# Performance work log

Hardware: AMD Instinct MI355X
Metric: run time of the kernel (lower is better)

Reference implementation:

```python
import jax, jax.numpy as jnp
import numpy as np

LOG_INV_TEMP = float(np.log(1.0 / 0.07))
B, N_IMG, N_GPS, G_DIM = 256, 49, 32, 256


def setup_inputs() -> dict:
    key = jax.random.key(0)
    k1, k2 = jax.random.split(key)
    return {
        "image_g_tokens": jax.random.normal(k1, (B, N_IMG, G_DIM), dtype=jnp.float32),
        "gps_g_tokens": jax.random.normal(k2, (B, N_GPS, G_DIM), dtype=jnp.float32),
        "logit_scale": jnp.asarray(LOG_INV_TEMP, dtype=jnp.float32),
    }


def _l2norm(x, eps=1e-12):
    # matches F.normalize(p=2, dim=-1)
    n = jnp.sqrt(jnp.sum(x * x, axis=-1, keepdims=True))
    return x / jnp.maximum(n, eps)


def _ce(logits, labels):
    # mean cross-entropy with integer labels
    logz = jax.nn.logsumexp(logits, axis=1)
    picked = jnp.take_along_axis(logits, labels[:, None], axis=1)[:, 0]
    return jnp.mean(logz - picked)


def reference(image_g_tokens, gps_g_tokens, logit_scale):
    img = _l2norm(image_g_tokens)   # (B, n, d)
    gps = _l2norm(gps_g_tokens)     # (B, m, d)
    # dist not initialized -> gather is identity, global == local
    scale = jnp.minimum(jnp.exp(logit_scale), 100.0)

    # token-level max-sim: (B, G, n, m) pairwise similarities
    sims_i2g = jnp.einsum('bnd,gmd->bgnm', img, gps)
    sims_g2i = jnp.einsum('bmd,gnd->bgmn', gps, img)
    logits_i2g = jnp.mean(jnp.max(sims_i2g, axis=3), axis=2) * scale  # (B, G)
    logits_g2i = jnp.mean(jnp.max(sims_g2i, axis=3), axis=2) * scale  # (B, G)

    labels = jnp.arange(img.shape[0])
    loss = (_ce(logits_i2g, labels) + _ce(logits_g2i, labels)) / 2.0
    return loss
```

## Files before the change

### kernel.cpp

```cpp
#include <hip/hip_runtime.h>

#define BB   256
#define NIMG 49
#define NGPS 32
#define DIM  256
#define MPAD 64

typedef __attribute__((ext_vector_type(8))) __bf16 bf16x8;
typedef __attribute__((ext_vector_type(4))) float  f32x4;
typedef __attribute__((ext_vector_type(4))) unsigned int u32x4;

__device__ inline unsigned short f2bf(float f) {
  unsigned int u = __float_as_uint(f);
  u += 0x7fff + ((u >> 16) & 1);
  return (unsigned short)(u >> 16);
}

template<int CTRL>
__device__ inline float dppmax(float v) {
  float o = __int_as_float(__builtin_amdgcn_update_dpp(0, __float_as_int(v), CTRL, 0xF, 0xF, true));
  return fmaxf(v, o);
}
template<int CTRL>
__device__ inline float dppadd(float v) {
  float o = __int_as_float(__builtin_amdgcn_update_dpp(0, __float_as_int(v), CTRL, 0xF, 0xF, true));
  return v + o;
}
__device__ inline float max16(float v) {
  v = dppmax<0xB1>(v); v = dppmax<0x4E>(v); v = dppmax<0x141>(v); v = dppmax<0x140>(v);
  return v;
}
__device__ inline float sum16(float v) {
  v = dppadd<0xB1>(v); v = dppadd<0x4E>(v); v = dppadd<0x141>(v); v = dppadd<0x140>(v);
  return v;
}

__global__ __launch_bounds__(256) void norm_kernel(
    const float* __restrict__ img, const float* __restrict__ gps,
    unsigned short* __restrict__ imgS, unsigned short* __restrict__ gpsS)
{
  int w    = (blockIdx.x * 256 + threadIdx.x) >> 6;
  int lane = threadIdx.x & 63;

  f32x4 x = (f32x4){0.f, 0.f, 0.f, 0.f};
  bool isimg; int b = 0, n = 0, g = 0, m = 0;
  if (w < BB * MPAD) {
    isimg = true; b = w >> 6; n = w & 63;
    if (n < NIMG)
      x = *reinterpret_cast<const f32x4*>(img + ((size_t)b * NIMG + n) * DIM + lane * 4);
  } else {
    isimg = false; int t = w - BB * MPAD; g = t >> 5; m = t & 31;
    x = *reinterpret_cast<const f32x4*>(gps + (size_t)t * DIM + lane * 4);
  }

  float ss = x[0]*x[0] + x[1]*x[1] + x[2]*x[2] + x[3]*x[3];
  #pragma unroll
  for (int d = 1; d < 64; d <<= 1) ss += __shfl_xor(ss, d);
  float inv = (ss > 0.f) ? (1.0f / fmaxf(sqrtf(ss), 1e-12f)) : 0.f;

  unsigned int w01 = (unsigned)f2bf(x[0]*inv) | ((unsigned)f2bf(x[1]*inv) << 16);
  unsigned int w23 = (unsigned)f2bf(x[2]*inv) | ((unsigned)f2bf(x[3]*inv) << 16);

  int L = lane;
  unsigned int a0 = __shfl(w01, 2 * L);
  unsigned int a1 = __shfl(w23, 2 * L);
  unsigned int a2 = __shfl(w01, 2 * L + 1);
  unsigned int a3 = __shfl(w23, 2 * L + 1);
  if (L < 32) {
    u32x4 v = {a0, a1, a2, a3};
    unsigned short* dst;
    if (isimg) {
      dst = imgS + (size_t)b * 16384 + L * 512 + n * 8;
    } else {
      int mt = m >> 4, c = m & 15, kc = L >> 2, grp = L & 3;
      dst = gpsS + (size_t)g * 8192 + mt * 4096 + kc * 512 + (grp * 16 + c) * 8;
    }
    *reinterpret_cast<u32x4*>(dst) = v;
  }
}

__global__ __launch_bounds__(256, 4) void pair_kernel(
    const unsigned short* __restrict__ imgS, const unsigned short* __restrict__ gpsS,
    float* __restrict__ i2g, float* __restrict__ g2i)
{
  int tid  = threadIdx.x;
  int wv   = tid >> 6;
  int lane = tid & 63;
  int c    = lane & 15, grp = lane >> 4;
  int b    = blockIdx.x >> 3, gc = blockIdx.x & 7;
  int wvu  = __builtin_amdgcn_readfirstlane(wv);

  __shared__ unsigned short As[MPAD * DIM];

  {
    const unsigned short* src = imgS + (size_t)b * 16384 + lane * 8;
    #pragma unroll
    for (int i = 0; i < 8; ++i) {
      int s = wvu * 8 + i;
      bf16x8 v = *reinterpret_cast<const bf16x8*>(src + s * 512);
      unsigned int rb = lane * 512;
      unsigned int sw = (lane & 7) << 4;
      *reinterpret_cast<bf16x8*>(reinterpret_cast<char*>(As) + ((rb + s * 16) ^ sw)) = v;
    }
  }
  __syncthreads();

  const char* Ab = reinterpret_cast<const char*>(As);
  unsigned int swr   = (c & 7) << 4;
  unsigned int abase = c * 512;

  const unsigned short* gb = gpsS + ((size_t)(gc * 32 + wvu * 8)) * 8192;
  unsigned int lane8 = lane * 8;

  #pragma unroll 1
  for (int st = 0; st < 4; ++st) {
    f32x4 acc[2][2][4];
    #pragma unroll
    for (int g = 0; g < 2; ++g)
      #pragma unroll
      for (int mt = 0; mt < 2; ++mt)
        #pragma unroll
        for (int hf = 0; hf < 4; ++hf)
          acc[g][mt][hf] = (f32x4){0.f, 0.f, 0.f, 0.f};

    #pragma unroll 2
    for (int kc = 0; kc < 8; ++kc) {
      const unsigned short* p = gb + kc * 512 + lane8;
      bf16x8 q00 = *reinterpret_cast<const bf16x8*>(p);
      bf16x8 q01 = *reinterpret_cast<const bf16x8*>(p + 4096);
      bf16x8 q10 = *reinterpret_cast<const bf16x8*>(p + 8192);
      bf16x8 q11 = *reinterpret_cast<const bf16x8*>(p + 12288);
      unsigned int off = ((unsigned)(grp * 16 + kc * 64)) ^ swr;
      const char* ab = Ab + abase + off;
      bf16x8 a0 = *reinterpret_cast<const bf16x8*>(ab);
      bf16x8 a1 = *reinterpret_cast<const bf16x8*>(ab + 8192);
      bf16x8 a2 = *reinterpret_cast<const bf16x8*>(ab + 16384);
      bf16x8 a3 = *reinterpret_cast<const bf16x8*>(ab + 24576);
      acc[0][0][0] = __builtin_amdgcn_mfma_f32_16x16x32_bf16(q00, a0, acc[0][0][0], 0, 0, 0);
      acc[0][0][1] = __builtin_amdgcn_mfma_f32_16x16x32_bf16(q00, a1, acc[0][0][1], 0, 0, 0);
      acc[0][0][2] = __builtin_amdgcn_mfma_f32_16x16x32_bf16(q00, a2, acc[0][0][2], 0, 0, 0);
      acc[0][0][3] = __builtin_amdgcn_mfma_f32_16x16x32_bf16(q00, a3, acc[0][0][3], 0, 0, 0);
      acc[0][1][0] = __builtin_amdgcn_mfma_f32_16x16x32_bf16(q01, a0, acc[0][1][0], 0, 0, 0);
      acc[0][1][1] = __builtin_amdgcn_mfma_f32_16x16x32_bf16(q01, a1, acc[0][1][1], 0, 0, 0);
      acc[0][1][2] = __builtin_amdgcn_mfma_f32_16x16x32_bf16(q01, a2, acc[0][1][2], 0, 0, 0);
      acc[0][1][3] = __builtin_amdgcn_mfma_f32_16x16x32_bf16(q01, a3, acc[0][1][3], 0, 0, 0);
      acc[1][0][0] = __builtin_amdgcn_mfma_f32_16x16x32_bf16(q10, a0, acc[1][0][0], 0, 0, 0);
      acc[1][0][1] = __builtin_amdgcn_mfma_f32_16x16x32_bf16(q10, a1, acc[1][0][1], 0, 0, 0);
      acc[1][0][2] = __builtin_amdgcn_mfma_f32_16x16x32_bf16(q10, a2, acc[1][0][2], 0, 0, 0);
      acc[1][0][3] = __builtin_amdgcn_mfma_f32_16x16x32_bf16(q10, a3, acc[1][0][3], 0, 0, 0);
      acc[1][1][0] = __builtin_amdgcn_mfma_f32_16x16x32_bf16(q11, a0, acc[1][1][0], 0, 0, 0);
      acc[1][1][1] = __builtin_amdgcn_mfma_f32_16x16x32_bf16(q11, a1, acc[1][1][1], 0, 0, 0);
      acc[1][1][2] = __builtin_amdgcn_mfma_f32_16x16x32_bf16(q11, a2, acc[1][1][2], 0, 0, 0);
      acc[1][1][3] = __builtin_amdgcn_mfma_f32_16x16x32_bf16(q11, a3, acc[1][1][3], 0, 0, 0);
    }

    #pragma unroll
    for (int g = 0; g < 2; ++g) {
      float vmax[4];
      #pragma unroll
      for (int hf = 0; hf < 4; ++hf) {
        float m0 = fmaxf(fmaxf(acc[g][0][hf][0], acc[g][0][hf][1]),
                         fmaxf(acc[g][0][hf][2], acc[g][0][hf][3]));
        float m1 = fmaxf(fmaxf(acc[g][1][hf][0], acc[g][1][hf][1]),
                         fmaxf(acc[g][1][hf][2], acc[g][1][hf][3]));
        float vm = fmaxf(m0, m1);
        vm = fmaxf(vm, __shfl_xor(vm, 16));
        vm = fmaxf(vm, __shfl_xor(vm, 32));
        vmax[hf] = vm;
      }
      float s = vmax[0] + vmax[1] + vmax[2] + ((c == 0) ? vmax[3] : 0.0f);
      s = sum16(s);

      float t = 0.f;
      #pragma unroll
      for (int mt = 0; mt < 2; ++mt)
        #pragma unroll
        for (int r = 0; r < 4; ++r) {
          float h3 = (c == 0) ? acc[g][mt][3][r] : -1.0e30f;
          float hm = fmaxf(fmaxf(acc[g][mt][0][r], acc[g][mt][1][r]),
                           fmaxf(acc[g][mt][2][r], h3));
          hm = max16(hm);
          t += hm;
        }
      t += __shfl_xor(t, 16);
      t += __shfl_xor(t, 32);

      if (lane == 0) {
        int gg = gc * 32 + wvu * 8 + st * 2 + g;
        i2g[b * 256 + gg] = s * (1.0f / NIMG);
        g2i[gg * 256 + b] = t * (1.0f / NGPS);
      }
    }
    gb += 16384;
  }
}

__global__ __launch_bounds__(256) void ce_kernel(
    const float* __restrict__ i2g, const float* __restrict__ g2i,
    const float* __restrict__ lsp, float* __restrict__ partial)
{
  int b = blockIdx.x, t = threadIdx.x, lane = t & 63, wv = t >> 6;
  float s = fminf(expf(lsp[0]), 100.0f);
  float v1 = s * i2g[b * 256 + t];
  float v2 = s * g2i[b * 256 + t];

  float m1 = v1, m2 = v2;
  #pragma unroll
  for (int d = 1; d < 64; d <<= 1) {
    m1 = fmaxf(m1, __shfl_xor(m1, d));
    m2 = fmaxf(m2, __shfl_xor(m2, d));
  }
  __shared__ float sm[2][4];
  if (lane == 0) { sm[0][wv] = m1; sm[1][wv] = m2; }
  __syncthreads();
  m1 = fmaxf(fmaxf(sm[0][0], sm[0][1]), fmaxf(sm[0][2], sm[0][3]));
  m2 = fmaxf(fmaxf(sm[1][0], sm[1][1]), fmaxf(sm[1][2], sm[1][3]));

  float e1 = expf(v1 - m1), e2 = expf(v2 - m2);
  #pragma unroll
  for (int d = 1; d < 64; d <<= 1) {
    e1 += __shfl_xor(e1, d);
    e2 += __shfl_xor(e2, d);
  }
  __shared__ float se[2][4];
  if (lane == 0) { se[0][wv] = e1; se[1][wv] = e2; }
  __syncthreads();
  if (t == 0) {
    float S1 = se[0][0] + se[0][1] + se[0][2] + se[0][3];
    float S2 = se[1][0] + se[1][1] + se[1][2] + se[1][3];
    float lse1 = m1 + logf(S1);
    float lse2 = m2 + logf(S2);
    partial[b] = (lse1 - s * i2g[b * 257]) + (lse2 - s * g2i[b * 257]);
  }
}

__global__ __launch_bounds__(256) void finish_kernel(
    const float* __restrict__ partial, float* __restrict__ out)
{
  int t = threadIdx.x, lane = t & 63, wv = t >> 6;
  float v = partial[t];
  #pragma unroll
  for (int d = 1; d < 64; d <<= 1) v += __shfl_xor(v, d);
  __shared__ float sp[4];
  if (lane == 0) sp[wv] = v;
  __syncthreads();
  if (t == 0) out[0] = (sp[0] + sp[1] + sp[2] + sp[3]) * (1.0f / 512.0f);
}

extern "C" void kernel_launch(void* const* d_in, const int* in_sizes, int n_in,
                              void* d_out, int out_size, void* d_ws, size_t ws_size,
                              hipStream_t stream)
{
  const float* img = (const float*)d_in[0];
  const float* gps = (const float*)d_in[1];
  const float* lsp = (const float*)d_in[2];
  float* out = (float*)d_out;
  char* ws = (char*)d_ws;

  unsigned short* imgS = (unsigned short*)(ws);
  unsigned short* gpsS = (unsigned short*)(ws + 8388608);
  float* i2g     = (float*)(ws + 12582912);
  float* g2i     = (float*)(ws + 12845056);
  float* partial = (float*)(ws + 13107200);

  norm_kernel<<<6144, 256, 0, stream>>>(img, gps, imgS, gpsS);
  pair_kernel<<<2048, 256, 0, stream>>>(imgS, gpsS, i2g, g2i);
  ce_kernel<<<256, 256, 0, stream>>>(i2g, g2i, lsp, partial);
  finish_kernel<<<1, 256, 0, stream>>>(partial, out);
}
```

Before: 87.09 us.

## Store image tokens in MFMA fragment layout and load directly from global

The normalization kernel now writes image tokens in a pre-swizzled MFMA operand layout. The pair kernel can then read A fragments straight from global memory (L2/L1) instead of staging a 32KB tile in LDS behind a barrier. This removes the LDS fill, the __syncthreads and the LDS reads. In exchange every wave re-reads the image tile from cache. The launch-bounds occupancy hint drops from 4 to 3 blocks per CU to give more register room for the extra in-flight global loads.

```diff
diff --git a/kernel.cpp b/kernel.cpp
--- a/kernel.cpp
+++ b/kernel.cpp
@@ -37,7 +37,7 @@
 
 __global__ __launch_bounds__(256) void norm_kernel(
     const float* __restrict__ img, const float* __restrict__ gps,
-    unsigned short* __restrict__ imgS, unsigned short* __restrict__ gpsS)
+    unsigned short* __restrict__ imgA, unsigned short* __restrict__ gpsS)
 {
   int w    = (blockIdx.x * 256 + threadIdx.x) >> 6;
   int lane = threadIdx.x & 63;
@@ -70,7 +70,8 @@
     u32x4 v = {a0, a1, a2, a3};
     unsigned short* dst;
     if (isimg) {
-      dst = imgS + (size_t)b * 16384 + L * 512 + n * 8;
+      dst = imgA + (size_t)b * 16384 + (L >> 2) * 2048 + (n >> 4) * 512
+                 + ((L & 3) * 16 + (n & 15)) * 8;
     } else {
       int mt = m >> 4, c = m & 15, kc = L >> 2, grp = L & 3;
       dst = gpsS + (size_t)g * 8192 + mt * 4096 + kc * 512 + (grp * 16 + c) * 8;
@@ -79,8 +80,8 @@
   }
 }
 
-__global__ __launch_bounds__(256, 4) void pair_kernel(
-    const unsigned short* __restrict__ imgS, const unsigned short* __restrict__ gpsS,
+__global__ __launch_bounds__(256, 3) void pair_kernel(
+    const unsigned short* __restrict__ imgA, const unsigned short* __restrict__ gpsS,
     float* __restrict__ i2g, float* __restrict__ g2i)
 {
   int tid  = threadIdx.x;
@@ -90,27 +91,9 @@
   int b    = blockIdx.x >> 3, gc = blockIdx.x & 7;
   int wvu  = __builtin_amdgcn_readfirstlane(wv);
 
-  __shared__ unsigned short As[MPAD * DIM];
-
-  {
-    const unsigned short* src = imgS + (size_t)b * 16384 + lane * 8;
-    #pragma unroll
-    for (int i = 0; i < 8; ++i) {
-      int s = wvu * 8 + i;
-      bf16x8 v = *reinterpret_cast<const bf16x8*>(src + s * 512);
-      unsigned int rb = lane * 512;
-      unsigned int sw = (lane & 7) << 4;
-      *reinterpret_cast<bf16x8*>(reinterpret_cast<char*>(As) + ((rb + s * 16) ^ sw)) = v;
-    }
-  }
-  __syncthreads();
-
-  const char* Ab = reinterpret_cast<const char*>(As);
-  unsigned int swr   = (c & 7) << 4;
-  unsigned int abase = c * 512;
-
+  unsigned int lane8 = lane * 8;
+  const unsigned short* pa = imgA + (size_t)b * 16384 + lane8;
   const unsigned short* gb = gpsS + ((size_t)(gc * 32 + wvu * 8)) * 8192;
-  unsigned int lane8 = lane * 8;
 
   #pragma unroll 1
   for (int st = 0; st < 4; ++st) {
@@ -130,12 +113,11 @@
       bf16x8 q01 = *reinterpret_cast<const bf16x8*>(p + 4096);
       bf16x8 q10 = *reinterpret_cast<const bf16x8*>(p + 8192);
       bf16x8 q11 = *reinterpret_cast<const bf16x8*>(p + 12288);
-      unsigned int off = ((unsigned)(grp * 16 + kc * 64)) ^ swr;
-      const char* ab = Ab + abase + off;
-      bf16x8 a0 = *reinterpret_cast<const bf16x8*>(ab);
-      bf16x8 a1 = *reinterpret_cast<const bf16x8*>(ab + 8192);
-      bf16x8 a2 = *reinterpret_cast<const bf16x8*>(ab + 16384);
-      bf16x8 a3 = *reinterpret_cast<const bf16x8*>(ab + 24576);
+      const unsigned short* ap = pa + kc * 2048;
+      bf16x8 a0 = *reinterpret_cast<const bf16x8*>(ap);
+      bf16x8 a1 = *reinterpret_cast<const bf16x8*>(ap + 512);
+      bf16x8 a2 = *reinterpret_cast<const bf16x8*>(ap + 1024);
+      bf16x8 a3 = *reinterpret_cast<const bf16x8*>(ap + 1536);
       acc[0][0][0] = __builtin_amdgcn_mfma_f32_16x16x32_bf16(q00, a0, acc[0][0][0], 0, 0, 0);
       acc[0][0][1] = __builtin_amdgcn_mfma_f32_16x16x32_bf16(q00, a1, acc[0][0][1], 0, 0, 0);
       acc[0][0][2] = __builtin_amdgcn_mfma_f32_16x16x32_bf16(q00, a2, acc[0][0][2], 0, 0, 0);
@@ -257,14 +239,14 @@
   float* out = (float*)d_out;
   char* ws = (char*)d_ws;
 
-  unsigned short* imgS = (unsigned short*)(ws);
+  unsigned short* imgA = (unsigned short*)(ws);
   unsigned short* gpsS = (unsigned short*)(ws + 8388608);
   float* i2g     = (float*)(ws + 12582912);
   float* g2i     = (float*)(ws + 12845056);
   float* partial = (float*)(ws + 13107200);
 
-  norm_kernel<<<6144, 256, 0, stream>>>(img, gps, imgS, gpsS);
-  pair_kernel<<<2048, 256, 0, stream>>>(imgS, gpsS, i2g, g2i);
+  norm_kernel<<<6144, 256, 0, stream>>>(img, gps, imgA, gpsS);
+  pair_kernel<<<2048, 256, 0, stream>>>(imgA, gpsS, i2g, g2i);
   ce_kernel<<<256, 256, 0, stream>>>(i2g, g2i, lsp, partial);
   finish_kernel<<<1, 256, 0, stream>>>(partial, out);
 }
```

Measured after the change: 96.61 us. +10.9%, slower.
